# Performance work log

Hardware: AMD Instinct MI355X
Metric: run time of the kernel (lower is better)

## Reference

```python
import jax, jax.numpy as jnp
import numpy as np

H, W = 2048, 2048
N = H * W
MEAN_MODULO = 1.0


def setup_inputs() -> dict:
    key = jax.random.key(0)
    k1, k2, k3 = jax.random.split(key, 3)
    pred_E = jax.random.uniform(k1, (N,), dtype=jnp.float32)
    pred_v = jax.random.uniform(k2, (N,), dtype=jnp.float32)
    strain = jax.random.normal(k3, (N, 3), dtype=jnp.float32)
    return {"pred_E": pred_E, "pred_v": pred_v, "strain": strain}


def _conv_valid(x_hw, k_33):
    # x_hw: [H, W] -> NHWC [1,H,W,1]; k_33: [3,3] -> HWIO [3,3,1,1]; cross-correlation, VALID
    x = x_hw[None, :, :, None]
    k = k_33[:, :, None, None]
    y = jax.lax.conv_general_dilated(
        x, k, window_strides=(1, 1), padding="VALID",
        dimension_numbers=("NHWC", "HWIO", "NHWC"))
    return y[0, :, :, 0]  # [H-2, W-2]


def reference(pred_E, pred_v, strain):
    # ---- calculate_stress (closed-form batched plane-stress constitutive law) ----
    v = pred_v
    e0, e1, e2 = strain[:, 0], strain[:, 1], strain[:, 2]
    # strain[i] @ [[1,v,0],[v,1,0],[0,0,(1-v)/2]]
    s0 = e0 + v * e1
    s1 = v * e0 + e1
    s2 = e2 * (1.0 - v) * 0.5
    frac = pred_E / (1.0 - v * v)          # E / (1 - v^2), broadcast over 3 components
    stress = jnp.stack([s0, s1, s2], axis=1) * frac[:, None]  # [N, 3]

    # ---- calculate_loss_r (FD equilibrium residuals via 3x3 stencils) ----
    sum_k = jnp.ones((3, 3), dtype=jnp.float32)
    wx_xx = jnp.array([[-1., -1., -1.], [0., 0., 0.], [1., 1., 1.]], dtype=jnp.float32)
    wx_xy = jnp.array([[1., 0., -1.], [1., 0., -1.], [1., 0., -1.]], dtype=jnp.float32)
    wy_yy = wx_xy
    wy_xy = wx_xx

    E_mat = pred_E.reshape(H, W)
    sxx = stress[:, 0].reshape(H, W)
    syy = stress[:, 1].reshape(H, W)
    sxy = stress[:, 2].reshape(H, W)

    E_conv = _conv_valid(E_mat, sum_k)
    fx = _conv_valid(sxx, wx_xx) + _conv_valid(sxy, wx_xy)
    fy = _conv_valid(syy, wy_yy) + _conv_valid(sxy, wy_xy)

    loss_x = jnp.mean(jnp.abs(fx / E_conv))
    loss_y = jnp.mean(jnp.abs(fy / E_conv))
    loss_e = jnp.abs(jnp.mean(pred_E) - MEAN_MODULO)
    return loss_x + loss_y + loss_e / 100.0
```

## Files before the change

### kernel.cpp

```cpp
#include <hip/hip_runtime.h>
#include <math.h>

#define HH 2048
#define WW 2048
#define TILE_H 32
#define TILE_W 64
#define ROWS 34
#define QC   17
#define LSTRIDE 72
#define NBLK (32 * 64)
#define NITEMS (ROWS * QC)

__device__ __forceinline__ float rcpf(float x) { return __builtin_amdgcn_rcpf(x); }

struct StageRegs {
    float4 E, V, A, B, C;
    int r, q;
    bool ld;
};

__device__ __forceinline__ void stage_load(
    const float* __restrict__ pred_E, const float* __restrict__ pred_v,
    const float* __restrict__ strain, int r0, int c0, int tid, StageRegs R[3])
{
    #pragma unroll
    for (int it = 0; it < 3; ++it) {
        const int idx = tid + it * 256;
        const int r = idx / QC;
        const int q = idx - r * QC;
        R[it].r = r; R[it].q = q;
        const int gi = r0 + r;
        const int gc = c0 + q * 4;
        const bool a = (idx < NITEMS) && (gi < HH) && (gc < WW);
        R[it].ld = a;
        if (a) {
            const int g = gi * WW + gc;
            R[it].E = *(const float4*)(pred_E + g);
            R[it].V = *(const float4*)(pred_v + g);
            const float* sp = strain + 3 * g;
            R[it].A = *(const float4*)(sp);
            R[it].B = *(const float4*)(sp + 4);
            R[it].C = *(const float4*)(sp + 8);
        }
    }
}

__device__ __forceinline__ void stage_math_store(
    StageRegs R[3], float& sumE,
    float (*sE)[LSTRIDE], float (*sxx)[LSTRIDE],
    float (*syy)[LSTRIDE], float (*sxy)[LSTRIDE])
{
    #pragma unroll
    for (int it = 0; it < 3; ++it) {
        if (R[it].ld) {
            const int r = R[it].r, q = R[it].q;
            const float e[4]  = {R[it].E.x, R[it].E.y, R[it].E.z, R[it].E.w};
            const float vv[4] = {R[it].V.x, R[it].V.y, R[it].V.z, R[it].V.w};
            const float s0[4] = {R[it].A.x, R[it].A.w, R[it].B.z, R[it].C.y};
            const float s1[4] = {R[it].A.y, R[it].B.x, R[it].B.w, R[it].C.z};
            const float s2[4] = {R[it].A.z, R[it].B.y, R[it].C.x, R[it].C.w};
            float xx[4], yy[4], xy[4];
            #pragma unroll
            for (int p = 0; p < 4; ++p) {
                const float v  = vv[p];
                const float fr = e[p] * rcpf(1.f - v * v);
                xx[p] = (s0[p] + v * s1[p]) * fr;
                yy[p] = (v * s0[p] + s1[p]) * fr;
                xy[p] = (s2[p] * (1.f - v) * 0.5f) * fr;
            }
            const int cq = 4 * q;
            *(float4*)&sE [r][cq] = R[it].E;
            *(float4*)&sxx[r][cq] = make_float4(xx[0], xx[1], xx[2], xx[3]);
            *(float4*)&syy[r][cq] = make_float4(yy[0], yy[1], yy[2], yy[3]);
            *(float4*)&sxy[r][cq] = make_float4(xy[0], xy[1], xy[2], xy[3]);
            if (r < TILE_H && q < 16)
                sumE += e[0] + e[1] + e[2] + e[3];
        }
    }
}

__device__ __forceinline__ void row7(
    int r, int tx, float* o,
    const float (*sE)[LSTRIDE], const float (*sxx)[LSTRIDE],
    const float (*syy)[LSTRIDE], const float (*sxy)[LSTRIDE])
{
    o[0] = sE [r][tx] + sE [r][tx + 1] + sE [r][tx + 2];
    o[1] = sxx[r][tx] + sxx[r][tx + 1] + sxx[r][tx + 2];
    const float l = sxy[r][tx], m = sxy[r][tx + 1], rg = sxy[r][tx + 2];
    o[2] = l + m + rg;
    o[3] = l;
    o[4] = rg;
    o[5] = syy[r][tx];
    o[6] = syy[r][tx + 2];
}

__device__ __forceinline__ void stencil(
    int r0, int c0, int tid, float& ax, float& ay,
    const float (*sE)[LSTRIDE], const float (*sxx)[LSTRIDE],
    const float (*syy)[LSTRIDE], const float (*sxy)[LSTRIDE])
{
    const int tx = tid & 63;
    const int ty = tid >> 6;
    const int lb = ty * 8;

    float w0[7], w1[7], w2[7];
    row7(lb + 0, tx, w0, sE, sxx, syy, sxy);
    row7(lb + 1, tx, w1, sE, sxx, syy, sxy);

    const bool cok = (c0 + tx) < (WW - 2);
    #pragma unroll
    for (int k = 0; k < 8; ++k) {
        row7(lb + k + 2, tx, w2, sE, sxx, syy, sxy);
        const int gi = r0 + lb + k;
        if (cok && gi < (HH - 2)) {
            const float rEc = rcpf(w0[0] + w1[0] + w2[0]);
            const float fx = (w2[1] - w0[1])
                           + (w0[3] + w1[3] + w2[3])
                           - (w0[4] + w1[4] + w2[4]);
            const float fy = (w0[5] + w1[5] + w2[5])
                           - (w0[6] + w1[6] + w2[6])
                           + (w2[2] - w0[2]);
            ax += fabsf(fx) * rEc;
            ay += fabsf(fy) * rEc;
        }
        #pragma unroll
        for (int j = 0; j < 7; ++j) { w0[j] = w1[j]; w1[j] = w2[j]; }
    }
}

__global__ __launch_bounds__(256, 4) void fused_loss_kernel(
    const float* __restrict__ pred_E,
    const float* __restrict__ pred_v,
    const float* __restrict__ strain,
    float* __restrict__ part)
{
    __shared__ float sE [ROWS][LSTRIDE];
    __shared__ float sxx[ROWS][LSTRIDE];
    __shared__ float syy[ROWS][LSTRIDE];
    __shared__ float sxy[ROWS][LSTRIDE];

    const int tid = threadIdx.x;
    const int r0 = blockIdx.y * TILE_H;
    const int c0 = blockIdx.x * TILE_W;

    float sumE = 0.f, ax = 0.f, ay = 0.f;
    StageRegs R[3];

    stage_load(pred_E, pred_v, strain, r0, c0, tid, R);
    stage_math_store(R, sumE, sE, sxx, syy, sxy);
    __syncthreads();
    stencil(r0, c0, tid, ax, ay, sE, sxx, syy, sxy);

    #pragma unroll
    for (int off = 32; off > 0; off >>= 1) {
        ax   += __shfl_down(ax, off);
        ay   += __shfl_down(ay, off);
        sumE += __shfl_down(sumE, off);
    }
    __shared__ float red[3][4];
    const int wave = tid >> 6, lane = tid & 63;
    __syncthreads();
    if (lane == 0) { red[0][wave] = ax; red[1][wave] = ay; red[2][wave] = sumE; }
    __syncthreads();
    if (tid == 0) {
        const int b = blockIdx.y * 32 + blockIdx.x;
        part[b]            = red[0][0] + red[0][1] + red[0][2] + red[0][3];
        part[NBLK + b]     = red[1][0] + red[1][1] + red[1][2] + red[1][3];
        part[2 * NBLK + b] = red[2][0] + red[2][1] + red[2][2] + red[2][3];
    }
}

__global__ __launch_bounds__(256) void finalize_kernel(
    const float* __restrict__ part, float* __restrict__ out)
{
    const int tid = threadIdx.x;
    const float4* px = (const float4*)(part);
    const float4* py = (const float4*)(part + NBLK);
    const float4* pe = (const float4*)(part + 2 * NBLK);
    float x = 0.f, y = 0.f, e = 0.f;
    #pragma unroll
    for (int k = 0; k < 2; ++k) {
        const int i = tid + k * 256;
        const float4 a = px[i], b = py[i], c = pe[i];
        x += a.x + a.y + a.z + a.w;
        y += b.x + b.y + b.z + b.w;
        e += c.x + c.y + c.z + c.w;
    }
    #pragma unroll
    for (int off = 32; off > 0; off >>= 1) {
        x += __shfl_down(x, off);
        y += __shfl_down(y, off);
        e += __shfl_down(e, off);
    }
    __shared__ float red[3][4];
    const int wave = tid >> 6, lane = tid & 63;
    if (lane == 0) { red[0][wave] = x; red[1][wave] = y; red[2][wave] = e; }
    __syncthreads();
    if (tid == 0) {
        const float rx = red[0][0] + red[0][1] + red[0][2] + red[0][3];
        const float ry = red[1][0] + red[1][1] + red[1][2] + red[1][3];
        const float re = red[2][0] + red[2][1] + red[2][2] + red[2][3];
        const float M = (float)((HH - 2) * (WW - 2));
        const float loss_x = rx / M;
        const float loss_y = ry / M;
        const float loss_e = fabsf(re / (float)(HH * WW) - 1.0f);
        out[0] = loss_x + loss_y + loss_e * 0.01f;
    }
}

extern "C" void kernel_launch(void* const* d_in, const int* in_sizes, int n_in,
                              void* d_out, int out_size, void* d_ws, size_t ws_size,
                              hipStream_t stream) {
    const float* pred_E = (const float*)d_in[0];
    const float* pred_v = (const float*)d_in[1];
    const float* strain = (const float*)d_in[2];
    float* out  = (float*)d_out;
    float* part = (float*)d_ws;

    dim3 grid(WW / TILE_W, HH / TILE_H);
    fused_loss_kernel<<<grid, 256, 0, stream>>>(pred_E, pred_v, strain, part);
    finalize_kernel<<<1, 256, 0, stream>>>(part, out);
}
```

Measured before the change: 108.9 us.

## Process two tiles per block with prefetch and fuse finalize via last-block ticket

Each block now handles two adjacent 32x64 tiles. Global loads for the second tile are issued before the first tile's stencil runs, so load latency overlaps stencil compute. The separate finalize kernel is removed: an atomic ticket lets the last block reduce all partials and write the output, saving a launch. The cost is doubled register staging (two StageRegs sets), which may lower occupancy, and a grid of 1024 blocks, which lowers parallelism.

```diff
diff --git a/kernel.cpp b/kernel.cpp
--- a/kernel.cpp
+++ b/kernel.cpp
@@ -8,10 +8,14 @@
 #define ROWS 34
 #define QC   17
 #define LSTRIDE 72
-#define NBLK (32 * 64)
+#define GRIDX 16
+#define GRIDY 64
+#define NBLOCKS (GRIDX * GRIDY)
 #define NITEMS (ROWS * QC)
 
 __device__ __forceinline__ float rcpf(float x) { return __builtin_amdgcn_rcpf(x); }
+
+__device__ int g_ticket = 0;
 
 struct StageRegs {
     float4 E, V, A, B, C;
@@ -132,24 +136,32 @@
     const float* __restrict__ pred_E,
     const float* __restrict__ pred_v,
     const float* __restrict__ strain,
-    float* __restrict__ part)
+    float* __restrict__ part,
+    float* __restrict__ out)
 {
     __shared__ float sE [ROWS][LSTRIDE];
     __shared__ float sxx[ROWS][LSTRIDE];
     __shared__ float syy[ROWS][LSTRIDE];
     __shared__ float sxy[ROWS][LSTRIDE];
+    __shared__ float red[3][4];
+    __shared__ int   is_last;
 
     const int tid = threadIdx.x;
     const int r0 = blockIdx.y * TILE_H;
-    const int c0 = blockIdx.x * TILE_W;
+    const int c0 = blockIdx.x * (2 * TILE_W);
 
     float sumE = 0.f, ax = 0.f, ay = 0.f;
-    StageRegs R[3];
-
-    stage_load(pred_E, pred_v, strain, r0, c0, tid, R);
-    stage_math_store(R, sumE, sE, sxx, syy, sxy);
-    __syncthreads();
+    StageRegs R0[3], R1[3];
+
+    stage_load(pred_E, pred_v, strain, r0, c0, tid, R0);
+    stage_math_store(R0, sumE, sE, sxx, syy, sxy);
+    __syncthreads();
+    stage_load(pred_E, pred_v, strain, r0, c0 + TILE_W, tid, R1);
     stencil(r0, c0, tid, ax, ay, sE, sxx, syy, sxy);
+    __syncthreads();
+    stage_math_store(R1, sumE, sE, sxx, syy, sxy);
+    __syncthreads();
+    stencil(r0, c0 + TILE_W, tid, ax, ay, sE, sxx, syy, sxy);
 
     #pragma unroll
     for (int off = 32; off > 0; off >>= 1) {
@@ -157,54 +169,46 @@
         ay   += __shfl_down(ay, off);
         sumE += __shfl_down(sumE, off);
     }
-    __shared__ float red[3][4];
     const int wave = tid >> 6, lane = tid & 63;
-    __syncthreads();
     if (lane == 0) { red[0][wave] = ax; red[1][wave] = ay; red[2][wave] = sumE; }
     __syncthreads();
     if (tid == 0) {
-        const int b = blockIdx.y * 32 + blockIdx.x;
-        part[b]            = red[0][0] + red[0][1] + red[0][2] + red[0][3];
-        part[NBLK + b]     = red[1][0] + red[1][1] + red[1][2] + red[1][3];
-        part[2 * NBLK + b] = red[2][0] + red[2][1] + red[2][2] + red[2][3];
-    }
-}
-
-__global__ __launch_bounds__(256) void finalize_kernel(
-    const float* __restrict__ part, float* __restrict__ out)
-{
-    const int tid = threadIdx.x;
-    const float4* px = (const float4*)(part);
-    const float4* py = (const float4*)(part + NBLK);
-    const float4* pe = (const float4*)(part + 2 * NBLK);
-    float x = 0.f, y = 0.f, e = 0.f;
-    #pragma unroll
-    for (int k = 0; k < 2; ++k) {
-        const int i = tid + k * 256;
-        const float4 a = px[i], b = py[i], c = pe[i];
-        x += a.x + a.y + a.z + a.w;
-        y += b.x + b.y + b.z + b.w;
-        e += c.x + c.y + c.z + c.w;
-    }
-    #pragma unroll
-    for (int off = 32; off > 0; off >>= 1) {
-        x += __shfl_down(x, off);
-        y += __shfl_down(y, off);
-        e += __shfl_down(e, off);
-    }
-    __shared__ float red[3][4];
-    const int wave = tid >> 6, lane = tid & 63;
-    if (lane == 0) { red[0][wave] = x; red[1][wave] = y; red[2][wave] = e; }
-    __syncthreads();
-    if (tid == 0) {
-        const float rx = red[0][0] + red[0][1] + red[0][2] + red[0][3];
-        const float ry = red[1][0] + red[1][1] + red[1][2] + red[1][3];
-        const float re = red[2][0] + red[2][1] + red[2][2] + red[2][3];
-        const float M = (float)((HH - 2) * (WW - 2));
-        const float loss_x = rx / M;
-        const float loss_y = ry / M;
-        const float loss_e = fabsf(re / (float)(HH * WW) - 1.0f);
-        out[0] = loss_x + loss_y + loss_e * 0.01f;
+        const int b = blockIdx.y * GRIDX + blockIdx.x;
+        part[b]               = red[0][0] + red[0][1] + red[0][2] + red[0][3];
+        part[NBLOCKS + b]     = red[1][0] + red[1][1] + red[1][2] + red[1][3];
+        part[2 * NBLOCKS + b] = red[2][0] + red[2][1] + red[2][2] + red[2][3];
+        __threadfence();
+        const int old = atomicAdd(&g_ticket, 1);
+        is_last = (old == NBLOCKS - 1);
+    }
+    __syncthreads();
+
+    if (is_last) {
+        __threadfence();
+        const float4* px = (const float4*)(part);
+        const float4* py = (const float4*)(part + NBLOCKS);
+        const float4* pe = (const float4*)(part + 2 * NBLOCKS);
+        const float4 a = px[tid], b2 = py[tid], c = pe[tid];
+        float x = a.x + a.y + a.z + a.w;
+        float y = b2.x + b2.y + b2.z + b2.w;
+        float e = c.x + c.y + c.z + c.w;
+        #pragma unroll
+        for (int off = 32; off > 0; off >>= 1) {
+            x += __shfl_down(x, off);
+            y += __shfl_down(y, off);
+            e += __shfl_down(e, off);
+        }
+        __syncthreads();
+        if (lane == 0) { red[0][wave] = x; red[1][wave] = y; red[2][wave] = e; }
+        __syncthreads();
+        if (tid == 0) {
+            const float rx = red[0][0] + red[0][1] + red[0][2] + red[0][3];
+            const float ry = red[1][0] + red[1][1] + red[1][2] + red[1][3];
+            const float re = red[2][0] + red[2][1] + red[2][2] + red[2][3];
+            const float M = (float)((HH - 2) * (WW - 2));
+            out[0] = rx / M + ry / M + fabsf(re / (float)(HH * WW) - 1.0f) * 0.01f;
+            atomicExch(&g_ticket, 0);
+        }
     }
 }
 
@@ -217,7 +221,6 @@
     float* out  = (float*)d_out;
     float* part = (float*)d_ws;
 
-    dim3 grid(WW / TILE_W, HH / TILE_H);
-    fused_loss_kernel<<<grid, 256, 0, stream>>>(pred_E, pred_v, strain, part);
-    finalize_kernel<<<1, 256, 0, stream>>>(part, out);
-}
+    dim3 grid(GRIDX, GRIDY);
+    fused_loss_kernel<<<grid, 256, 0, stream>>>(pred_E, pred_v, strain, part, out);
+}
```

New measurement: 142.1 us. 30.4% more time.
